# Kernel optimization log

Hardware: AMD Instinct MI355X
Metric: run time of the kernel (lower is better)

## Reference

```python
import jax, jax.numpy as jnp
import numpy as np

T, B, D, H, F, O = 256, 512, 256, 512, 64, 1


def setup_inputs() -> dict:
    key = jax.random.key(0)
    ks = jax.random.split(key, 16)
    s = 0.05
    return {
        "inputs": jax.random.normal(ks[0], (T, B, D), jnp.float32),
        "hidden_init": jnp.zeros((B, H), jnp.float32),
        "cell_init": jnp.zeros((B, H), jnp.float32),
        # LSTMCell params (torch gate order: i, f, g, o)
        "W_ih": jax.random.normal(ks[1], (4 * H, D), jnp.float32) * s,
        "W_hh": jax.random.normal(ks[2], (4 * H, H), jnp.float32) * s,
        "b_ih": jax.random.normal(ks[3], (4 * H,), jnp.float32) * s,
        "b_hh": jax.random.normal(ks[4], (4 * H,), jnp.float32) * s,
        # Attention fc: hidden_dim -> 1
        "attn_w": jax.random.normal(ks[5], (1, H), jnp.float32) * s,
        "attn_b": jax.random.normal(ks[6], (1,), jnp.float32) * s,
        # Output MLP: H->F, F->F, F->F//2, F//2->O
        "W1": jax.random.normal(ks[7], (F, H), jnp.float32) * s,
        "b1": jax.random.normal(ks[8], (F,), jnp.float32) * s,
        "W2": jax.random.normal(ks[9], (F, F), jnp.float32) * s,
        "b2": jax.random.normal(ks[10], (F,), jnp.float32) * s,
        "W3": jax.random.normal(ks[11], (F // 2, F), jnp.float32) * s,
        "b3": jax.random.normal(ks[12], (F // 2,), jnp.float32) * s,
        "W4": jax.random.normal(ks[13], (O, F // 2), jnp.float32) * s,
        "b4": jax.random.normal(ks[14], (O,), jnp.float32) * s,
    }


def _lstm_scan(inputs, h0, c0, W_ih, W_hh, b_ih, b_hh):
    def step(carry, x):
        h, c = carry
        gates = x @ W_ih.T + b_ih + h @ W_hh.T + b_hh  # (B, 4H)
        i, f, g, o = jnp.split(gates, 4, axis=-1)
        c = jax.nn.sigmoid(f) * c + jax.nn.sigmoid(i) * jnp.tanh(g)
        h = jax.nn.sigmoid(o) * jnp.tanh(c)
        return (h, c), h

    (hT, cT), hs = jax.lax.scan(step, (h0, c0), inputs)
    return hT, cT, hs  # hs: (T, B, H)


def reference(inputs, hidden_init, cell_init, W_ih, W_hh, b_ih, b_hh,
              attn_w, attn_b, W1, b1, W2, b2, W3, b3, W4, b4):
    hT, cT, hs = _lstm_scan(inputs, hidden_init, cell_init, W_ih, W_hh, b_ih, b_hh)
    hs = jnp.transpose(hs, (1, 0, 2))            # (B, T, H) == torch.stack(hiddens, dim=1)
    scores = hs @ attn_w.T + attn_b              # (B, T, 1)
    weights = jax.nn.softmax(scores, axis=1)     # softmax over time
    context = jnp.sum(weights * hs, axis=1)      # (B, H)
    x = jnp.tanh(context @ W1.T + b1)
    x = jnp.tanh(x @ W2.T + b2)
    x = jnp.tanh(x @ W3.T + b3)
    out = x @ W4.T + b4                          # (B, O)
    return out, hT, cT
```

## Files before the change

kernel.cpp:

```cpp
#include <hip/hip_runtime.h>


typedef _Float16 f16x8 __attribute__((ext_vector_type(8)));
typedef short    s16x8 __attribute__((ext_vector_type(8)));
typedef float    f32x4 __attribute__((ext_vector_type(4)));

union F16U { f16x8 v; _Float16 e[8]; };

__device__ __forceinline__ float h2f(unsigned short b) {
    return (float)__builtin_bit_cast(_Float16, b);
}
__device__ __forceinline__ unsigned short f2h(float f) {
    return __builtin_bit_cast(unsigned short, (_Float16)f);
}
__device__ __forceinline__ float sigf(float x) { return 1.0f / (1.0f + __expf(-x)); }
__device__ __forceinline__ float tanh_(float x) {
    float e = __expf(-2.0f * fabsf(x));
    float r = (1.0f - e) / (1.0f + e);
    return x < 0.0f ? -r : r;
}
__device__ __forceinline__ unsigned umin_(unsigned a, unsigned b) { return a < b ? a : b; }

__device__ __forceinline__ f16x8 loadA32(const float* p) {
    float4 a = *(const float4*)p, b = *(const float4*)(p + 4);
    F16U r;
    r.e[0]=(_Float16)a.x; r.e[1]=(_Float16)a.y; r.e[2]=(_Float16)a.z; r.e[3]=(_Float16)a.w;
    r.e[4]=(_Float16)b.x; r.e[5]=(_Float16)b.y; r.e[6]=(_Float16)b.z; r.e[7]=(_Float16)b.w;
    return r.v;
}

#define MFMA16(a, b, c) __builtin_amdgcn_mfma_f32_16x16x32_f16((a), (b), (c), 0, 0, 0)
#define BIDX(g, kc) (((g) * 16 + lj) * 96 + ((((kc) * 4) + lq) ^ vg[(g)]))

__device__ __forceinline__ void issue_x(const float* x_t, int arow, int lq, float4* xpf) {
    const float* xb = x_t + (size_t)arow * 256 + lq * 8;
#pragma unroll
    for (int i = 0; i < 8; ++i) {
        asm volatile("global_load_dwordx4 %0, %1, off offset:%c2"
                     : "=v"(xpf[2 * i]) : "v"(xb), "i"(i * 128));
        asm volatile("global_load_dwordx4 %0, %1, off offset:%c2"
                     : "=v"(xpf[2 * i + 1]) : "v"(xb), "i"(i * 128 + 16));
    }
}

__device__ __forceinline__ void gemm_x_reg(const float4* xpf, const f16x8* Wl,
    int lj, int lq, const int* vg,
    f32x4& acc0, f32x4& acc1, f32x4& acc2, f32x4& acc3)
{
    asm volatile("s_waitcnt vmcnt(0)" ::: "memory");
    __builtin_amdgcn_sched_barrier(0);
#pragma unroll
    for (int kc = 0; kc < 8; ++kc) {
        float4 a = xpf[2 * kc], b = xpf[2 * kc + 1];
        F16U r;
        r.e[0]=(_Float16)a.x; r.e[1]=(_Float16)a.y; r.e[2]=(_Float16)a.z; r.e[3]=(_Float16)a.w;
        r.e[4]=(_Float16)b.x; r.e[5]=(_Float16)b.y; r.e[6]=(_Float16)b.z; r.e[7]=(_Float16)b.w;
        acc0 = MFMA16(r.v, Wl[BIDX(0, kc)], acc0);
        acc1 = MFMA16(r.v, Wl[BIDX(1, kc)], acc1);
        acc2 = MFMA16(r.v, Wl[BIDX(2, kc)], acc2);
        acc3 = MFMA16(r.v, Wl[BIDX(3, kc)], acc3);
    }
}

__device__ __forceinline__ void wait_flags(const uint4* fbase, int l, unsigned target) {
    if (l < 32) {
        const uint4* p = fbase + l;
        unsigned m;
        do {
            uint4 v;
            asm volatile("global_load_dwordx4 %0, %1, off sc0 sc1" : "=v"(v) : "v"(p));
            asm volatile("s_waitcnt vmcnt(0)" ::: "memory");
            m = umin_(umin_(v.x, v.y), umin_(v.z, v.w));
        } while (m < target);
    }
    __builtin_amdgcn_sched_barrier(0);
}

__device__ __forceinline__ void gemm_h_ic(const unsigned short* hsrc, const f16x8* Wl,
    int arow, int lj, int lq, const int* vg,
    const unsigned short* ap_dot, const unsigned short* ap_ctx,
    uint4& hdot, uint2& hctx,
    f32x4& acc0, f32x4& acc1, f32x4& acc2, f32x4& acc3)
{
    const unsigned short* hp = hsrc + (size_t)arow * 512 + lq * 8;
    s16x8 hf[16];
#pragma unroll
    for (int i = 0; i < 16; ++i)
        asm volatile("global_load_dwordx4 %0, %1, off offset:%c2 sc0 sc1"
                     : "=v"(hf[i]) : "v"(hp), "i"(i * 64));
    asm volatile("global_load_dwordx4 %0, %1, off sc0 sc1" : "=v"(hdot) : "v"(ap_dot));
    asm volatile("global_load_dwordx2 %0, %1, off sc0 sc1" : "=v"(hctx) : "v"(ap_ctx));

    asm volatile("s_waitcnt vmcnt(10)" ::: "memory");
    __builtin_amdgcn_sched_barrier(0);
#pragma unroll
    for (int kc = 8; kc < 16; ++kc) {
        f16x8 a = __builtin_bit_cast(f16x8, hf[kc - 8]);
        acc0 = MFMA16(a, Wl[BIDX(0, kc)], acc0);
        acc1 = MFMA16(a, Wl[BIDX(1, kc)], acc1);
        acc2 = MFMA16(a, Wl[BIDX(2, kc)], acc2);
        acc3 = MFMA16(a, Wl[BIDX(3, kc)], acc3);
    }
    asm volatile("s_waitcnt vmcnt(2)" ::: "memory");
    __builtin_amdgcn_sched_barrier(0);
#pragma unroll
    for (int kc = 16; kc < 24; ++kc) {
        f16x8 a = __builtin_bit_cast(f16x8, hf[kc - 8]);
        acc0 = MFMA16(a, Wl[BIDX(0, kc)], acc0);
        acc1 = MFMA16(a, Wl[BIDX(1, kc)], acc1);
        acc2 = MFMA16(a, Wl[BIDX(2, kc)], acc2);
        acc3 = MFMA16(a, Wl[BIDX(3, kc)], acc3);
    }
}

__device__ __forceinline__ void gemm_h_init(const float* hsrc, const f16x8* Wl,
    int arow, int lj, int lq, const int* vg,
    f32x4& acc0, f32x4& acc1, f32x4& acc2, f32x4& acc3)
{
    const float* hb = hsrc + (size_t)arow * 512 + lq * 8;
#pragma unroll
    for (int kc = 8; kc < 24; ++kc) {
        f16x8 a = loadA32(hb + (kc - 8) * 32);
        acc0 = MFMA16(a, Wl[BIDX(0, kc)], acc0);
        acc1 = MFMA16(a, Wl[BIDX(1, kc)], acc1);
        acc2 = MFMA16(a, Wl[BIDX(2, kc)], acc2);
        acc3 = MFMA16(a, Wl[BIDX(3, kc)], acc3);
    }
}

__device__ __forceinline__ void attn_apply(uint4 hd, uint2 hc, const float* wv8,
    float s_bias, float& m_r, float& l_r, float ctx[4])
{
    float p = h2f((unsigned short)(hd.x & 0xffffu)) * wv8[0]
            + h2f((unsigned short)(hd.x >> 16))     * wv8[1]
            + h2f((unsigned short)(hd.y & 0xffffu)) * wv8[2]
            + h2f((unsigned short)(hd.y >> 16))     * wv8[3]
            + h2f((unsigned short)(hd.z & 0xffffu)) * wv8[4]
            + h2f((unsigned short)(hd.z >> 16))     * wv8[5]
            + h2f((unsigned short)(hd.w & 0xffffu)) * wv8[6]
            + h2f((unsigned short)(hd.w >> 16))     * wv8[7];
#pragma unroll
    for (int off = 32; off > 0; off >>= 1) p += __shfl_xor(p, off);
    float s = p + s_bias;
    float m_new = fmaxf(m_r, s);
    float scale = __expf(m_r - m_new);
    float pr    = __expf(s - m_new);
    ctx[0] = ctx[0] * scale + pr * h2f((unsigned short)(hc.x & 0xffffu));
    ctx[1] = ctx[1] * scale + pr * h2f((unsigned short)(hc.x >> 16));
    ctx[2] = ctx[2] * scale + pr * h2f((unsigned short)(hc.y & 0xffffu));
    ctx[3] = ctx[3] * scale + pr * h2f((unsigned short)(hc.y >> 16));
    l_r = l_r * scale + pr;
    m_r = m_new;
}

#define SMEM_BYTES 104192

__global__ __launch_bounds__(256, 1) void lstm_persist(
    const float* __restrict__ xg,
    const float* __restrict__ hinit, const float* __restrict__ cinit,
    const float* __restrict__ W_ih, const float* __restrict__ W_hh,
    const float* __restrict__ b_ih, const float* __restrict__ b_hh,
    const float* __restrict__ attn_w, const float* __restrict__ attn_b,
    const float* __restrict__ W1, const float* __restrict__ b1,
    const float* __restrict__ W2, const float* __restrict__ b2,
    const float* __restrict__ W3, const float* __restrict__ b3,
    const float* __restrict__ W4, const float* __restrict__ b4,
    float* __restrict__ out,
    unsigned short* __restrict__ hb0, unsigned short* __restrict__ hb1,
    unsigned* __restrict__ flags)
{
    extern __shared__ char smem[];
    f16x8* Wl    = (f16x8*)smem;
    float* bsum  = (float*)(smem + 98304);
    float* xmlp  = (float*)(smem + 98304 + 512);
    float* x1s   = xmlp + 1024;
    float* x2s   = x1s + 128;
    float* x3s   = x2s + 128;

    const int tid = threadIdx.x, bid = blockIdx.x;
    const int mt = bid & 7, nt = bid >> 3;
    const int hc0 = nt * 16;
    const int w = tid >> 6, l = tid & 63;
    const int lj = l & 15, lq = l >> 4;

    int vg[4];
#pragma unroll
    for (int g = 0; g < 4; ++g) {
        int q = g * 16 + lj;
        vg[g] = ((q >> 3) ^ q) & 7;
    }

    {
        int q = tid >> 2, si = tid & 3;
        int vq = ((q >> 3) ^ q) & 7;
        int grow = (q >> 4) * 512 + hc0 + (q & 15);
        const float* ih = W_ih + (size_t)grow * 256;
        const float* hh = W_hh + (size_t)grow * 512;
        for (int cc = 0; cc < 24; ++cc) {
            int s = si * 24 + cc;
            int k0 = s * 8;
            const float* p = (k0 < 256) ? (ih + k0) : (hh + (k0 - 256));
            float4 a = *(const float4*)p, b = *(const float4*)(p + 4);
            F16U r;
            r.e[0]=(_Float16)a.x; r.e[1]=(_Float16)a.y; r.e[2]=(_Float16)a.z; r.e[3]=(_Float16)a.w;
            r.e[4]=(_Float16)b.x; r.e[5]=(_Float16)b.y; r.e[6]=(_Float16)b.z; r.e[7]=(_Float16)b.w;
            Wl[q * 96 + (s ^ vq)] = r.v;
        }
        if (tid < 64) {
            int gr = (tid >> 4) * 512 + hc0 + (tid & 15);
            bsum[tid] = b_ih[gr] + b_hh[gr];
        }
    }
    __syncthreads();

    const int arow = mt * 64 + w * 16 + lj;
    const int crow = mt * 64 + w * 16 + lq * 4;
    const int ccol = hc0 + lj;
    float creg[4];
#pragma unroll
    for (int r = 0; r < 4; ++r)
        creg[r] = cinit[(size_t)(crow + r) * 512 + ccol];

    float m_r = -__builtin_inff(), l_r = 0.f;
    float ctx[4] = {0.f, 0.f, 0.f, 0.f};
    uint4 hdot = {0, 0, 0, 0}; uint2 hctx = {0, 0};
    const int attr0 = mt * 64 + nt * 2;
    const int arow_at = attr0 + (w >> 1);
    const float s_bias = attn_b[0];
    float wv8[8];
    {
        float4 a = *(const float4*)(attn_w + l * 8);
        float4 b = *(const float4*)(attn_w + l * 8 + 4);
        wv8[0]=a.x; wv8[1]=a.y; wv8[2]=a.z; wv8[3]=a.w;
        wv8[4]=b.x; wv8[5]=b.y; wv8[6]=b.z; wv8[7]=b.w;
    }
    float bs0 = bsum[lj], bs1 = bsum[16 + lj], bs2 = bsum[32 + lj], bs3 = bsum[48 + lj];

    const size_t aoff_dot = (size_t)arow_at * 512 + l * 8;
    const size_t aoff_ctx = (size_t)arow_at * 512 + (w & 1) * 256 + l * 4;
    const uint4* fbase = (const uint4*)flags + mt * 32;
    unsigned* myflag = flags + (size_t)(mt * 32 + nt) * 4 + w;

    float4 xpf[16];
    issue_x(xg, arow, lq, xpf);

    for (int t = 0; t < 256; ++t) {
        unsigned short* hb_cur = (t & 1) ? hb1 : hb0;
        const unsigned short* hb_prev = (t & 1) ? hb0 : hb1;

        f32x4 acc0 = {0,0,0,0}, acc1 = {0,0,0,0}, acc2 = {0,0,0,0}, acc3 = {0,0,0,0};
        gemm_x_reg(xpf, Wl, lj, lq, vg, acc0, acc1, acc2, acc3);

        if (t >= 2) attn_apply(hdot, hctx, wv8, s_bias, m_r, l_r, ctx);

        if (t > 0) {
            wait_flags(fbase, l, (unsigned)t);
            gemm_h_ic(hb_prev, Wl, arow, lj, lq, vg,
                      hb_prev + aoff_dot, hb_prev + aoff_ctx, hdot, hctx,
                      acc0, acc1, acc2, acc3);
        } else {
            gemm_h_init(hinit, Wl, arow, lj, lq, vg, acc0, acc1, acc2, acc3);
        }

#pragma unroll
        for (int r = 0; r < 4; ++r) {
            float ii = sigf(acc0[r] + bs0);
            float ff = sigf(acc1[r] + bs1);
            float gt = tanh_(acc2[r] + bs2);
            float oo = sigf(acc3[r] + bs3);
            float cn = ff * creg[r] + ii * gt;
            creg[r] = cn;
            float hv = oo * tanh_(cn);
            size_t off = (size_t)(crow + r) * 512 + ccol;
            unsigned short hvs = f2h(hv);
            unsigned short* sp = hb_cur + off;
            asm volatile("global_store_short %0, %1, off sc0 sc1"
                         :: "v"(sp), "v"(hvs) : "memory");
            if (t == 255) out[512 + off] = hv;
        }

        const float* xnext = xg + (size_t)(t < 255 ? t + 1 : 255) * 131072;
        issue_x(xnext, arow, lq, xpf);

        asm volatile("s_waitcnt vmcnt(16)" ::: "memory");
        if (l == 0) {
            unsigned fv = (unsigned)(t + 1);
            asm volatile("global_store_dword %0, %1, off sc0 sc1"
                         :: "v"(myflag), "v"(fv) : "memory");
        }
    }

    attn_apply(hdot, hctx, wv8, s_bias, m_r, l_r, ctx);
    wait_flags(fbase, l, 256u);
    {
        const unsigned short* hp = hb1 + aoff_dot;
        const unsigned short* hc = hb1 + aoff_ctx;
        asm volatile("global_load_dwordx4 %0, %1, off sc0 sc1" : "=v"(hdot) : "v"(hp));
        asm volatile("global_load_dwordx2 %0, %1, off sc0 sc1" : "=v"(hctx) : "v"(hc));
        asm volatile("s_waitcnt vmcnt(0)" ::: "memory");
        __builtin_amdgcn_sched_barrier(0);
        attn_apply(hdot, hctx, wv8, s_bias, m_r, l_r, ctx);
    }

#pragma unroll
    for (int r = 0; r < 4; ++r)
        out[512 + 262144 + (size_t)(crow + r) * 512 + ccol] = creg[r];

    {
        float linv = 1.0f / l_r;
        int row = tid >> 7, coff = (tid & 127) * 4;
#pragma unroll
        for (int i = 0; i < 4; ++i) xmlp[row * 512 + coff + i] = ctx[i] * linv;
    }
    __syncthreads();
    if (tid < 128) {
        int r = tid >> 6, f = tid & 63;
        const float* wp = W1 + (size_t)f * 512;
        const float* xp = xmlp + r * 512;
        float a = b1[f];
        for (int j = 0; j < 512; ++j) a = fmaf(xp[j], wp[j], a);
        x1s[r * 64 + f] = tanh_(a);
    }
    __syncthreads();
    if (tid < 128) {
        int r = tid >> 6, f = tid & 63;
        const float* wp = W2 + f * 64;
        const float* xp = x1s + r * 64;
        float a = b2[f];
        for (int j = 0; j < 64; ++j) a = fmaf(xp[j], wp[j], a);
        x2s[r * 64 + f] = tanh_(a);
    }
    __syncthreads();
    if (tid < 64) {
        int r = tid >> 5, f = tid & 31;
        const float* wp = W3 + f * 64;
        const float* xp = x2s + r * 64;
        float a = b3[f];
        for (int j = 0; j < 64; ++j) a = fmaf(xp[j], wp[j], a);
        x3s[r * 32 + f] = tanh_(a);
    }
    __syncthreads();
    if (tid < 2) {
        const float* xp = x3s + tid * 32;
        float a = b4[0];
        for (int j = 0; j < 32; ++j) a = fmaf(xp[j], W4[j], a);
        out[attr0 + tid] = a;
    }
}

extern "C" void kernel_launch(void* const* d_in, const int* in_sizes, int n_in,
                              void* d_out, int out_size, void* d_ws, size_t ws_size,
                              hipStream_t stream) {
    const float* xg     = (const float*)d_in[0];
    const float* hinit  = (const float*)d_in[1];
    const float* cinit  = (const float*)d_in[2];
    const float* W_ih   = (const float*)d_in[3];
    const float* W_hh   = (const float*)d_in[4];
    const float* b_ih   = (const float*)d_in[5];
    const float* b_hh   = (const float*)d_in[6];
    const float* attn_w = (const float*)d_in[7];
    const float* attn_b = (const float*)d_in[8];
    const float* W1 = (const float*)d_in[9],  *b1 = (const float*)d_in[10];
    const float* W2 = (const float*)d_in[11], *b2 = (const float*)d_in[12];
    const float* W3 = (const float*)d_in[13], *b3 = (const float*)d_in[14];
    const float* W4 = (const float*)d_in[15], *b4 = (const float*)d_in[16];

    unsigned short* hb0 = (unsigned short*)d_ws;
    unsigned short* hb1 = hb0 + 262144;
    unsigned* flags = (unsigned*)((char*)d_ws + 1048576);

    hipMemsetAsync(flags, 0, 4096, stream);
    hipFuncSetAttribute((const void*)lstm_persist,
                        hipFuncAttributeMaxDynamicSharedMemorySize, SMEM_BYTES);
    lstm_persist<<<256, 256, SMEM_BYTES, stream>>>(
        xg, hinit, cinit, W_ih, W_hh, b_ih, b_hh, attn_w, attn_b,
        W1, b1, W2, b2, W3, b3, W4, b4,
        (float*)d_out, hb0, hb1, flags);
}
```

Baseline: 1.698 ms.

## Keep LSTM weights in registers and store full hidden history per step

```diff
diff --git a/kernel.cpp b/kernel.cpp
--- a/kernel.cpp
+++ b/kernel.cpp
@@ -30,7 +30,6 @@
 }
 
 #define MFMA16(a, b, c) __builtin_amdgcn_mfma_f32_16x16x32_f16((a), (b), (c), 0, 0, 0)
-#define BIDX(g, kc) (((g) * 16 + lj) * 96 + ((((kc) * 4) + lq) ^ vg[(g)]))
 
 __device__ __forceinline__ void issue_x(const float* x_t, int arow, int lq, float4* xpf) {
     const float* xb = x_t + (size_t)arow * 256 + lq * 8;
@@ -43,22 +42,14 @@
     }
 }
 
-__device__ __forceinline__ void gemm_x_reg(const float4* xpf, const f16x8* Wl,
-    int lj, int lq, const int* vg,
-    f32x4& acc0, f32x4& acc1, f32x4& acc2, f32x4& acc3)
-{
-    asm volatile("s_waitcnt vmcnt(0)" ::: "memory");
-    __builtin_amdgcn_sched_barrier(0);
+__device__ __forceinline__ void cvt8(const float4* xpf, f16x8* xf) {
 #pragma unroll
     for (int kc = 0; kc < 8; ++kc) {
         float4 a = xpf[2 * kc], b = xpf[2 * kc + 1];
         F16U r;
         r.e[0]=(_Float16)a.x; r.e[1]=(_Float16)a.y; r.e[2]=(_Float16)a.z; r.e[3]=(_Float16)a.w;
         r.e[4]=(_Float16)b.x; r.e[5]=(_Float16)b.y; r.e[6]=(_Float16)b.z; r.e[7]=(_Float16)b.w;
-        acc0 = MFMA16(r.v, Wl[BIDX(0, kc)], acc0);
-        acc1 = MFMA16(r.v, Wl[BIDX(1, kc)], acc1);
-        acc2 = MFMA16(r.v, Wl[BIDX(2, kc)], acc2);
-        acc3 = MFMA16(r.v, Wl[BIDX(3, kc)], acc3);
+        xf[kc] = r.v;
     }
 }
 
@@ -74,58 +65,6 @@
         } while (m < target);
     }
     __builtin_amdgcn_sched_barrier(0);
-}
-
-__device__ __forceinline__ void gemm_h_ic(const unsigned short* hsrc, const f16x8* Wl,
-    int arow, int lj, int lq, const int* vg,
-    const unsigned short* ap_dot, const unsigned short* ap_ctx,
-    uint4& hdot, uint2& hctx,
-    f32x4& acc0, f32x4& acc1, f32x4& acc2, f32x4& acc3)
-{
-    const unsigned short* hp = hsrc + (size_t)arow * 512 + lq * 8;
-    s16x8 hf[16];
-#pragma unroll
-    for (int i = 0; i < 16; ++i)
-        asm volatile("global_load_dwordx4 %0, %1, off offset:%c2 sc0 sc1"
-                     : "=v"(hf[i]) : "v"(hp), "i"(i * 64));
-    asm volatile("global_load_dwordx4 %0, %1, off sc0 sc1" : "=v"(hdot) : "v"(ap_dot));
-    asm volatile("global_load_dwordx2 %0, %1, off sc0 sc1" : "=v"(hctx) : "v"(ap_ctx));
-
-    asm volatile("s_waitcnt vmcnt(10)" ::: "memory");
-    __builtin_amdgcn_sched_barrier(0);
-#pragma unroll
-    for (int kc = 8; kc < 16; ++kc) {
-        f16x8 a = __builtin_bit_cast(f16x8, hf[kc - 8]);
-        acc0 = MFMA16(a, Wl[BIDX(0, kc)], acc0);
-        acc1 = MFMA16(a, Wl[BIDX(1, kc)], acc1);
-        acc2 = MFMA16(a, Wl[BIDX(2, kc)], acc2);
-        acc3 = MFMA16(a, Wl[BIDX(3, kc)], acc3);
-    }
-    asm volatile("s_waitcnt vmcnt(2)" ::: "memory");
-    __builtin_amdgcn_sched_barrier(0);
-#pragma unroll
-    for (int kc = 16; kc < 24; ++kc) {
-        f16x8 a = __builtin_bit_cast(f16x8, hf[kc - 8]);
-        acc0 = MFMA16(a, Wl[BIDX(0, kc)], acc0);
-        acc1 = MFMA16(a, Wl[BIDX(1, kc)], acc1);
-        acc2 = MFMA16(a, Wl[BIDX(2, kc)], acc2);
-        acc3 = MFMA16(a, Wl[BIDX(3, kc)], acc3);
-    }
-}
-
-__device__ __forceinline__ void gemm_h_init(const float* hsrc, const f16x8* Wl,
-    int arow, int lj, int lq, const int* vg,
-    f32x4& acc0, f32x4& acc1, f32x4& acc2, f32x4& acc3)
-{
-    const float* hb = hsrc + (size_t)arow * 512 + lq * 8;
-#pragma unroll
-    for (int kc = 8; kc < 24; ++kc) {
-        f16x8 a = loadA32(hb + (kc - 8) * 32);
-        acc0 = MFMA16(a, Wl[BIDX(0, kc)], acc0);
-        acc1 = MFMA16(a, Wl[BIDX(1, kc)], acc1);
-        acc2 = MFMA16(a, Wl[BIDX(2, kc)], acc2);
-        acc3 = MFMA16(a, Wl[BIDX(3, kc)], acc3);
-    }
 }
 
 __device__ __forceinline__ void attn_apply(uint4 hd, uint2 hc, const float* wv8,
@@ -153,9 +92,10 @@
     m_r = m_new;
 }
 
-#define SMEM_BYTES 104192
-
-__global__ __launch_bounds__(256, 1) void lstm_persist(
+#define GSTRIDE 68
+#define SMEM_BYTES 24576
+
+__global__ __launch_bounds__(256, 1) void lstm_wreg(
     const float* __restrict__ xg,
     const float* __restrict__ hinit, const float* __restrict__ cinit,
     const float* __restrict__ W_ih, const float* __restrict__ W_hh,
@@ -166,60 +106,56 @@
     const float* __restrict__ W3, const float* __restrict__ b3,
     const float* __restrict__ W4, const float* __restrict__ b4,
     float* __restrict__ out,
-    unsigned short* __restrict__ hb0, unsigned short* __restrict__ hb1,
-    unsigned* __restrict__ flags)
+    unsigned short* __restrict__ hs, unsigned* __restrict__ flags)
 {
     extern __shared__ char smem[];
-    f16x8* Wl    = (f16x8*)smem;
-    float* bsum  = (float*)(smem + 98304);
-    float* xmlp  = (float*)(smem + 98304 + 512);
-    float* x1s   = xmlp + 1024;
-    float* x2s   = x1s + 128;
-    float* x3s   = x2s + 128;
+    float* gbuf = (float*)smem;
+    float* bsum = (float*)(smem + 17408);
+    float* xmlp = (float*)(smem + 17664);
+    float* x1s  = xmlp + 1024;
+    float* x2s  = x1s + 128;
+    float* x3s  = x2s + 128;
 
     const int tid = threadIdx.x, bid = blockIdx.x;
     const int mt = bid & 7, nt = bid >> 3;
     const int hc0 = nt * 16;
     const int w = tid >> 6, l = tid & 63;
     const int lj = l & 15, lq = l >> 4;
-
-    int vg[4];
-#pragma unroll
-    for (int g = 0; g < 4; ++g) {
-        int q = g * 16 + lj;
-        vg[g] = ((q >> 3) ^ q) & 7;
-    }
-
+    const int gA = (w & 1) * 2;
+    const int rh = (w >> 1) * 32;
+
+    if (tid < 64) {
+        int gr = (tid >> 4) * 512 + hc0 + (tid & 15);
+        bsum[tid] = b_ih[gr] + b_hh[gr];
+    }
+
+    f16x8 WA0[24], WA1[24];
     {
-        int q = tid >> 2, si = tid & 3;
-        int vq = ((q >> 3) ^ q) & 7;
-        int grow = (q >> 4) * 512 + hc0 + (q & 15);
-        const float* ih = W_ih + (size_t)grow * 256;
-        const float* hh = W_hh + (size_t)grow * 512;
-        for (int cc = 0; cc < 24; ++cc) {
-            int s = si * 24 + cc;
-            int k0 = s * 8;
-            const float* p = (k0 < 256) ? (ih + k0) : (hh + (k0 - 256));
-            float4 a = *(const float4*)p, b = *(const float4*)(p + 4);
-            F16U r;
-            r.e[0]=(_Float16)a.x; r.e[1]=(_Float16)a.y; r.e[2]=(_Float16)a.z; r.e[3]=(_Float16)a.w;
-            r.e[4]=(_Float16)b.x; r.e[5]=(_Float16)b.y; r.e[6]=(_Float16)b.z; r.e[7]=(_Float16)b.w;
-            Wl[q * 96 + (s ^ vq)] = r.v;
-        }
-        if (tid < 64) {
-            int gr = (tid >> 4) * 512 + hc0 + (tid & 15);
-            bsum[tid] = b_ih[gr] + b_hh[gr];
-        }
-    }
-    __syncthreads();
-
-    const int arow = mt * 64 + w * 16 + lj;
-    const int crow = mt * 64 + w * 16 + lq * 4;
-    const int ccol = hc0 + lj;
+        int wr0 = gA * 512 + hc0 + lj;
+        int wr1 = (gA + 1) * 512 + hc0 + lj;
+        const float* i0 = W_ih + (size_t)wr0 * 256 + lq * 8;
+        const float* h0 = W_hh + (size_t)wr0 * 512 + lq * 8;
+        const float* i1 = W_ih + (size_t)wr1 * 256 + lq * 8;
+        const float* h1 = W_hh + (size_t)wr1 * 512 + lq * 8;
+#pragma unroll
+        for (int kc = 0; kc < 8; ++kc) {
+            WA0[kc] = loadA32(i0 + kc * 32);
+            WA1[kc] = loadA32(i1 + kc * 32);
+        }
+#pragma unroll
+        for (int kc = 8; kc < 24; ++kc) {
+            WA0[kc] = loadA32(h0 + (kc - 8) * 32);
+            WA1[kc] = loadA32(h1 + (kc - 8) * 32);
+        }
+    }
+    __syncthreads();
+
+    const int hcol = tid & 15, rowq = tid >> 4;
     float creg[4];
 #pragma unroll
-    for (int r = 0; r < 4; ++r)
-        creg[r] = cinit[(size_t)(crow + r) * 512 + ccol];
+    for (int rr = 0; rr < 4; ++rr)
+        creg[rr] = cinit[(size_t)(mt * 64 + rowq * 4 + rr) * 512 + hc0 + hcol];
+    float bsI = bsum[hcol], bsF = bsum[16 + hcol], bsG = bsum[32 + hcol], bsO = bsum[48 + hcol];
 
     float m_r = -__builtin_inff(), l_r = 0.f;
     float ctx[4] = {0.f, 0.f, 0.f, 0.f};
@@ -234,44 +170,111 @@
         wv8[0]=a.x; wv8[1]=a.y; wv8[2]=a.z; wv8[3]=a.w;
         wv8[4]=b.x; wv8[5]=b.y; wv8[6]=b.z; wv8[7]=b.w;
     }
-    float bs0 = bsum[lj], bs1 = bsum[16 + lj], bs2 = bsum[32 + lj], bs3 = bsum[48 + lj];
-
     const size_t aoff_dot = (size_t)arow_at * 512 + l * 8;
     const size_t aoff_ctx = (size_t)arow_at * 512 + (w & 1) * 256 + l * 4;
     const uint4* fbase = (const uint4*)flags + mt * 32;
     unsigned* myflag = flags + (size_t)(mt * 32 + nt) * 4 + w;
 
-    float4 xpf[16];
-    issue_x(xg, arow, lq, xpf);
+    const int brow0 = mt * 64 + rh + lj;
+    const int brow1 = brow0 + 16;
 
     for (int t = 0; t < 256; ++t) {
-        unsigned short* hb_cur = (t & 1) ? hb1 : hb0;
-        const unsigned short* hb_prev = (t & 1) ? hb0 : hb1;
-
-        f32x4 acc0 = {0,0,0,0}, acc1 = {0,0,0,0}, acc2 = {0,0,0,0}, acc3 = {0,0,0,0};
-        gemm_x_reg(xpf, Wl, lj, lq, vg, acc0, acc1, acc2, acc3);
+        unsigned short* hb_cur = hs + (size_t)t * 262144;
+        const unsigned short* hb_prev = hb_cur - 262144;
+        const float* xt = xg + (size_t)t * 131072;
+
+        float4 xpf0[16], xpf1[16];
+        issue_x(xt, brow0, lq, xpf0);
+        issue_x(xt, brow1, lq, xpf1);
 
         if (t >= 2) attn_apply(hdot, hctx, wv8, s_bias, m_r, l_r, ctx);
+        if (t > 0) wait_flags(fbase, l, (unsigned)t);
+
+        asm volatile("s_waitcnt vmcnt(0)" ::: "memory");
+        __builtin_amdgcn_sched_barrier(0);
+        f16x8 xf0[8], xf1[8];
+        cvt8(xpf0, xf0);
+        cvt8(xpf1, xf1);
+
+        f32x4 a00 = {0,0,0,0}, a10 = {0,0,0,0}, a01 = {0,0,0,0}, a11 = {0,0,0,0};
+#pragma unroll
+        for (int kc = 0; kc < 8; ++kc) {
+            a00 = MFMA16(WA0[kc], xf0[kc], a00);
+            a10 = MFMA16(WA1[kc], xf0[kc], a10);
+            a01 = MFMA16(WA0[kc], xf1[kc], a01);
+            a11 = MFMA16(WA1[kc], xf1[kc], a11);
+        }
 
         if (t > 0) {
-            wait_flags(fbase, l, (unsigned)t);
-            gemm_h_ic(hb_prev, Wl, arow, lj, lq, vg,
-                      hb_prev + aoff_dot, hb_prev + aoff_ctx, hdot, hctx,
-                      acc0, acc1, acc2, acc3);
+            asm volatile("global_load_dwordx4 %0, %1, off" : "=v"(hdot) : "v"(hb_prev + aoff_dot));
+            asm volatile("global_load_dwordx2 %0, %1, off" : "=v"(hctx) : "v"(hb_prev + aoff_ctx));
+            s16x8 hf[16];
+            const unsigned short* hp0 = hb_prev + (size_t)brow0 * 512 + lq * 8;
+#pragma unroll
+            for (int i = 0; i < 16; ++i)
+                asm volatile("global_load_dwordx4 %0, %1, off offset:%c2"
+                             : "=v"(hf[i]) : "v"(hp0), "i"(i * 64));
+            asm volatile("s_waitcnt vmcnt(0)" ::: "memory");
+            __builtin_amdgcn_sched_barrier(0);
+#pragma unroll
+            for (int kc = 0; kc < 16; ++kc) {
+                f16x8 b = __builtin_bit_cast(f16x8, hf[kc]);
+                a00 = MFMA16(WA0[8 + kc], b, a00);
+                a10 = MFMA16(WA1[8 + kc], b, a10);
+            }
+            const unsigned short* hp1 = hb_prev + (size_t)brow1 * 512 + lq * 8;
+#pragma unroll
+            for (int i = 0; i < 16; ++i)
+                asm volatile("global_load_dwordx4 %0, %1, off offset:%c2"
+                             : "=v"(hf[i]) : "v"(hp1), "i"(i * 64));
+            asm volatile("s_waitcnt vmcnt(0)" ::: "memory");
+            __builtin_amdgcn_sched_barrier(0);
+#pragma unroll
+            for (int kc = 0; kc < 16; ++kc) {
+                f16x8 b = __builtin_bit_cast(f16x8, hf[kc]);
+                a01 = MFMA16(WA0[8 + kc], b, a01);
+                a11 = MFMA16(WA1[8 + kc], b, a11);
+            }
         } else {
-            gemm_h_init(hinit, Wl, arow, lj, lq, vg, acc0, acc1, acc2, acc3);
-        }
-
-#pragma unroll
-        for (int r = 0; r < 4; ++r) {
-            float ii = sigf(acc0[r] + bs0);
-            float ff = sigf(acc1[r] + bs1);
-            float gt = tanh_(acc2[r] + bs2);
-            float oo = sigf(acc3[r] + bs3);
-            float cn = ff * creg[r] + ii * gt;
-            creg[r] = cn;
+            const float* hb0p = hinit + (size_t)brow0 * 512 + lq * 8;
+            const float* hb1p = hinit + (size_t)brow1 * 512 + lq * 8;
+#pragma unroll
+            for (int kc = 0; kc < 16; ++kc) {
+                f16x8 b0 = loadA32(hb0p + kc * 32);
+                f16x8 b1 = loadA32(hb1p + kc * 32);
+                a00 = MFMA16(WA0[8 + kc], b0, a00);
+                a10 = MFMA16(WA1[8 + kc], b0, a10);
+                a01 = MFMA16(WA0[8 + kc], b1, a01);
+                a11 = MFMA16(WA1[8 + kc], b1, a11);
+            }
+        }
+
+        {
+            int r0 = (rh + lj) * GSTRIDE + gA * 17 + lq * 4;
+            int r1 = (rh + 16 + lj) * GSTRIDE + gA * 17 + lq * 4;
+#pragma unroll
+            for (int r = 0; r < 4; ++r) {
+                gbuf[r0 + r]      = a00[r];
+                gbuf[r0 + 17 + r] = a10[r];
+                gbuf[r1 + r]      = a01[r];
+                gbuf[r1 + 17 + r] = a11[r];
+            }
+        }
+        __syncthreads();
+
+#pragma unroll
+        for (int rr = 0; rr < 4; ++rr) {
+            int row = rowq * 4 + rr;
+            int base = row * GSTRIDE + hcol;
+            float vi = gbuf[base]      + bsI;
+            float vf = gbuf[base + 17] + bsF;
+            float vg = gbuf[base + 34] + bsG;
+            float vo = gbuf[base + 51] + bsO;
+            float ii = sigf(vi), ff = sigf(vf), gt = tanh_(vg), oo = sigf(vo);
+            float cn = ff * creg[rr] + ii * gt;
+            creg[rr] = cn;
             float hv = oo * tanh_(cn);
-            size_t off = (size_t)(crow + r) * 512 + ccol;
+            size_t off = (size_t)(mt * 64 + row) * 512 + hc0 + hcol;
             unsigned short hvs = f2h(hv);
             unsigned short* sp = hb_cur + off;
             asm volatile("global_store_short %0, %1, off sc0 sc1"
@@ -279,32 +282,29 @@
             if (t == 255) out[512 + off] = hv;
         }
 
-        const float* xnext = xg + (size_t)(t < 255 ? t + 1 : 255) * 131072;
-        issue_x(xnext, arow, lq, xpf);
-
-        asm volatile("s_waitcnt vmcnt(16)" ::: "memory");
+        asm volatile("s_waitcnt vmcnt(0)" ::: "memory");
         if (l == 0) {
             unsigned fv = (unsigned)(t + 1);
             asm volatile("global_store_dword %0, %1, off sc0 sc1"
                          :: "v"(myflag), "v"(fv) : "memory");
         }
+        __syncthreads();
     }
 
     attn_apply(hdot, hctx, wv8, s_bias, m_r, l_r, ctx);
     wait_flags(fbase, l, 256u);
     {
-        const unsigned short* hp = hb1 + aoff_dot;
-        const unsigned short* hc = hb1 + aoff_ctx;
-        asm volatile("global_load_dwordx4 %0, %1, off sc0 sc1" : "=v"(hdot) : "v"(hp));
-        asm volatile("global_load_dwordx2 %0, %1, off sc0 sc1" : "=v"(hctx) : "v"(hc));
+        const unsigned short* hlast = hs + (size_t)255 * 262144;
+        asm volatile("global_load_dwordx4 %0, %1, off" : "=v"(hdot) : "v"(hlast + aoff_dot));
+        asm volatile("global_load_dwordx2 %0, %1, off" : "=v"(hctx) : "v"(hlast + aoff_ctx));
         asm volatile("s_waitcnt vmcnt(0)" ::: "memory");
         __builtin_amdgcn_sched_barrier(0);
         attn_apply(hdot, hctx, wv8, s_bias, m_r, l_r, ctx);
     }
 
 #pragma unroll
-    for (int r = 0; r < 4; ++r)
-        out[512 + 262144 + (size_t)(crow + r) * 512 + ccol] = creg[r];
+    for (int rr = 0; rr < 4; ++rr)
+        out[512 + 262144 + (size_t)(mt * 64 + rowq * 4 + rr) * 512 + hc0 + hcol] = creg[rr];
 
     {
         float linv = 1.0f / l_r;
@@ -365,15 +365,15 @@
     const float* W3 = (const float*)d_in[13], *b3 = (const float*)d_in[14];
     const float* W4 = (const float*)d_in[15], *b4 = (const float*)d_in[16];
 
-    unsigned short* hb0 = (unsigned short*)d_ws;
-    unsigned short* hb1 = hb0 + 262144;
-    unsigned* flags = (unsigned*)((char*)d_ws + 1048576);
+    const size_t HS_BYTES = 134217728ull;
+    unsigned short* hs = (unsigned short*)d_ws;
+    unsigned* flags = (unsigned*)((char*)d_ws + HS_BYTES);
 
     hipMemsetAsync(flags, 0, 4096, stream);
-    hipFuncSetAttribute((const void*)lstm_persist,
+    hipFuncSetAttribute((const void*)lstm_wreg,
                         hipFuncAttributeMaxDynamicSharedMemorySize, SMEM_BYTES);
-    lstm_persist<<<256, 256, SMEM_BYTES, stream>>>(
+    lstm_wreg<<<256, 256, SMEM_BYTES, stream>>>(
         xg, hinit, cinit, W_ih, W_hh, b_ih, b_hh, attn_w, attn_b,
         W1, b1, W2, b2, W3, b3, W4, b4,
-        (float*)d_out, hb0, hb1, flags);
-}
+        (float*)d_out, hs, flags);
+}
```

Measured after the change: 2.563 ms. 51.0% more time.

## Store full hidden-state history to drop coherence bits on h loads

Applied to the files above, without the earlier changes.

```diff
diff --git a/kernel.cpp b/kernel.cpp
--- a/kernel.cpp
+++ b/kernel.cpp
@@ -30,7 +30,7 @@
 }
 
 #define MFMA16(a, b, c) __builtin_amdgcn_mfma_f32_16x16x32_f16((a), (b), (c), 0, 0, 0)
-#define BIDX(g, kc) (((g) * 16 + lj) * 96 + ((((kc) * 4) + lq) ^ vg[(g)]))
+#define BIDX(g, kc)  (((g) * 16 + lj) * 96 + ((((kc) * 4) + lq) ^ vg[(g)]))
 
 __device__ __forceinline__ void issue_x(const float* x_t, int arow, int lq, float4* xpf) {
     const float* xb = x_t + (size_t)arow * 256 + lq * 8;
@@ -76,7 +76,7 @@
     __builtin_amdgcn_sched_barrier(0);
 }
 
-__device__ __forceinline__ void gemm_h_ic(const unsigned short* hsrc, const f16x8* Wl,
+__device__ __forceinline__ void gemm_h_fb(const unsigned short* hsrc, const f16x8* Wl,
     int arow, int lj, int lq, const int* vg,
     const unsigned short* ap_dot, const unsigned short* ap_ctx,
     uint4& hdot, uint2& hctx,
@@ -86,10 +86,10 @@
     s16x8 hf[16];
 #pragma unroll
     for (int i = 0; i < 16; ++i)
-        asm volatile("global_load_dwordx4 %0, %1, off offset:%c2 sc0 sc1"
+        asm volatile("global_load_dwordx4 %0, %1, off offset:%c2"
                      : "=v"(hf[i]) : "v"(hp), "i"(i * 64));
-    asm volatile("global_load_dwordx4 %0, %1, off sc0 sc1" : "=v"(hdot) : "v"(ap_dot));
-    asm volatile("global_load_dwordx2 %0, %1, off sc0 sc1" : "=v"(hctx) : "v"(ap_ctx));
+    asm volatile("global_load_dwordx4 %0, %1, off" : "=v"(hdot) : "v"(ap_dot));
+    asm volatile("global_load_dwordx2 %0, %1, off" : "=v"(hctx) : "v"(ap_ctx));
 
     asm volatile("s_waitcnt vmcnt(10)" ::: "memory");
     __builtin_amdgcn_sched_barrier(0);
@@ -113,7 +113,7 @@
     }
 }
 
-__device__ __forceinline__ void gemm_h_init(const float* hsrc, const f16x8* Wl,
+__device__ __forceinline__ void gemm_h_init_fb(const float* hsrc, const f16x8* Wl,
     int arow, int lj, int lq, const int* vg,
     f32x4& acc0, f32x4& acc1, f32x4& acc2, f32x4& acc3)
 {
@@ -153,9 +153,9 @@
     m_r = m_new;
 }
 
-#define SMEM_BYTES 104192
-
-__global__ __launch_bounds__(256, 1) void lstm_persist(
+#define SMEM_FB 104192
+
+__global__ __launch_bounds__(256, 1) void lstm_hist(
     const float* __restrict__ xg,
     const float* __restrict__ hinit, const float* __restrict__ cinit,
     const float* __restrict__ W_ih, const float* __restrict__ W_hh,
@@ -166,8 +166,7 @@
     const float* __restrict__ W3, const float* __restrict__ b3,
     const float* __restrict__ W4, const float* __restrict__ b4,
     float* __restrict__ out,
-    unsigned short* __restrict__ hb0, unsigned short* __restrict__ hb1,
-    unsigned* __restrict__ flags)
+    unsigned short* __restrict__ hbA, unsigned* __restrict__ flags)
 {
     extern __shared__ char smem[];
     f16x8* Wl    = (f16x8*)smem;
@@ -200,11 +199,7 @@
             int s = si * 24 + cc;
             int k0 = s * 8;
             const float* p = (k0 < 256) ? (ih + k0) : (hh + (k0 - 256));
-            float4 a = *(const float4*)p, b = *(const float4*)(p + 4);
-            F16U r;
-            r.e[0]=(_Float16)a.x; r.e[1]=(_Float16)a.y; r.e[2]=(_Float16)a.z; r.e[3]=(_Float16)a.w;
-            r.e[4]=(_Float16)b.x; r.e[5]=(_Float16)b.y; r.e[6]=(_Float16)b.z; r.e[7]=(_Float16)b.w;
-            Wl[q * 96 + (s ^ vq)] = r.v;
+            Wl[q * 96 + (s ^ vq)] = loadA32(p);
         }
         if (tid < 64) {
             int gr = (tid >> 4) * 512 + hc0 + (tid & 15);
@@ -245,8 +240,8 @@
     issue_x(xg, arow, lq, xpf);
 
     for (int t = 0; t < 256; ++t) {
-        unsigned short* hb_cur = (t & 1) ? hb1 : hb0;
-        const unsigned short* hb_prev = (t & 1) ? hb0 : hb1;
+        unsigned short* hb_cur = hbA + (size_t)t * 262144;
+        const unsigned short* hb_prev = hb_cur - 262144;
 
         f32x4 acc0 = {0,0,0,0}, acc1 = {0,0,0,0}, acc2 = {0,0,0,0}, acc3 = {0,0,0,0};
         gemm_x_reg(xpf, Wl, lj, lq, vg, acc0, acc1, acc2, acc3);
@@ -255,11 +250,11 @@
 
         if (t > 0) {
             wait_flags(fbase, l, (unsigned)t);
-            gemm_h_ic(hb_prev, Wl, arow, lj, lq, vg,
+            gemm_h_fb(hb_prev, Wl, arow, lj, lq, vg,
                       hb_prev + aoff_dot, hb_prev + aoff_ctx, hdot, hctx,
                       acc0, acc1, acc2, acc3);
         } else {
-            gemm_h_init(hinit, Wl, arow, lj, lq, vg, acc0, acc1, acc2, acc3);
+            gemm_h_init_fb(hinit, Wl, arow, lj, lq, vg, acc0, acc1, acc2, acc3);
         }
 
 #pragma unroll
@@ -293,10 +288,11 @@
     attn_apply(hdot, hctx, wv8, s_bias, m_r, l_r, ctx);
     wait_flags(fbase, l, 256u);
     {
-        const unsigned short* hp = hb1 + aoff_dot;
-        const unsigned short* hc = hb1 + aoff_ctx;
-        asm volatile("global_load_dwordx4 %0, %1, off sc0 sc1" : "=v"(hdot) : "v"(hp));
-        asm volatile("global_load_dwordx2 %0, %1, off sc0 sc1" : "=v"(hctx) : "v"(hc));
+        const unsigned short* hlast = hbA + (size_t)255 * 262144;
+        const unsigned short* hp = hlast + aoff_dot;
+        const unsigned short* hc = hlast + aoff_ctx;
+        asm volatile("global_load_dwordx4 %0, %1, off" : "=v"(hdot) : "v"(hp));
+        asm volatile("global_load_dwordx2 %0, %1, off" : "=v"(hctx) : "v"(hc));
         asm volatile("s_waitcnt vmcnt(0)" ::: "memory");
         __builtin_amdgcn_sched_barrier(0);
         attn_apply(hdot, hctx, wv8, s_bias, m_r, l_r, ctx);
@@ -365,15 +361,15 @@
     const float* W3 = (const float*)d_in[13], *b3 = (const float*)d_in[14];
     const float* W4 = (const float*)d_in[15], *b4 = (const float*)d_in[16];
 
-    unsigned short* hb0 = (unsigned short*)d_ws;
-    unsigned short* hb1 = hb0 + 262144;
-    unsigned* flags = (unsigned*)((char*)d_ws + 1048576);
-
+    const size_t HS_BYTES = 134217728ull;
+
+    unsigned short* hs = (unsigned short*)d_ws;
+    unsigned* flags = (unsigned*)((char*)d_ws + HS_BYTES);
     hipMemsetAsync(flags, 0, 4096, stream);
-    hipFuncSetAttribute((const void*)lstm_persist,
-                        hipFuncAttributeMaxDynamicSharedMemorySize, SMEM_BYTES);
-    lstm_persist<<<256, 256, SMEM_BYTES, stream>>>(
+    hipFuncSetAttribute((const void*)lstm_hist,
+                        hipFuncAttributeMaxDynamicSharedMemorySize, SMEM_FB);
+    lstm_hist<<<256, 256, SMEM_FB, stream>>>(
         xg, hinit, cinit, W_ih, W_hh, b_ih, b_hh, attn_w, attn_b,
         W1, b1, W2, b2, W3, b3, W4, b4,
-        (float*)d_out, hb0, hb1, flags);
-}
+        (float*)d_out, hs, flags);
+}
```

Result: faster. 1.588 ms (median of 2 runs) (-6.5%).
